# Kernel optimization log

Measured on AMD Instinct MI355X. Metric: run time of the kernel, lower is better.

The kernel has to match this reference:

```python
import jax, jax.numpy as jnp
import numpy as np

H = 16        # num heads
ALPHA = 1.3   # entmax alpha
N_ITER = 50   # bisection iterations
EPS = 1e-5    # layernorm eps


def entmax_bisect(x, alpha=ALPHA, n_iter=N_ITER):
    # x: (..., K). Bisection entmax along last axis (Peters et al. 2019).
    am1 = alpha - 1.0
    x = x - jnp.max(x, axis=-1, keepdims=True)
    m = jnp.max(x, axis=-1, keepdims=True)  # == 0 after shift
    lo, hi = m - 10.0, m + 10.0
    def step(carry, _):
        lo, hi = carry
        mid = 0.5 * (lo + hi)
        p = jnp.maximum(am1 * x - mid, 0.0) ** (1.0 / am1)
        gt = jnp.sum(p, axis=-1, keepdims=True) > 1.0
        return (jnp.where(gt, mid, lo), jnp.where(gt, hi, mid)), None
    (lo, hi), _ = jax.lax.scan(jax.checkpoint(step), (lo, hi), None, length=n_iter)
    p = jnp.maximum(am1 * x - hi, 0.0) ** (1.0 / am1)
    return p / (jnp.sum(p, axis=-1, keepdims=True) + 1e-12)


def _heads(t, B, N, hd):
    return t.reshape(B, N, H, hd).transpose(0, 2, 1, 3)  # (B,H,N,hd)


def attn_branch(x, mask, wq, bq, wk, bk, wv, bv, wo, bo, use_entmax):
    B, N, D = x.shape
    hd = D // H
    q = _heads(x @ wq + bq, B, N, hd)
    k = _heads(x @ wk + bk, B, N, hd)
    v = _heads(x @ wv + bv, B, N, hd)
    s = jnp.einsum('bhqd,bhkd->bhqk', q, k) / float(np.sqrt(hd)) + mask
    if use_entmax:
        s = s - jnp.max(s, axis=-1, keepdims=True)
        a = entmax_bisect(s)
    else:
        a = jax.nn.softmax(s, axis=-1)
    o = jnp.einsum('bhqk,bhkd->bhqd', a, v).transpose(0, 2, 1, 3).reshape(B, N, D)
    return o @ wo + bo


def layer_norm(x, g, b):
    m = jnp.mean(x, axis=-1, keepdims=True)
    v = jnp.mean((x - m) ** 2, axis=-1, keepdims=True)
    return (x - m) * jax.lax.rsqrt(v + EPS) * g + b


def setup_inputs():
    B, N, D, F, FILM, NMODS = 4, 512, 2048, 8192, 64, 10000
    key = jax.random.key(0)
    ks = iter(jax.random.split(key, 64))
    rn = lambda *s: jax.random.normal(next(ks), s, dtype=jnp.float32)
    inp = dict(
        x=rn(B, N, D),
        attn_mask_intra=jnp.zeros((N, N), jnp.float32),
        attn_mask_inter=jnp.zeros((N, N), jnp.float32),
        mods=jax.random.randint(next(ks), (B, N), 0, 9999),
        film_emb=rn(NMODS, FILM) * 0.02,
        film_gw=rn(FILM, D) * 0.02, film_gb=jnp.zeros((D,), jnp.float32),
        film_bw=rn(FILM, D) * 0.02, film_bb=jnp.zeros((D,), jnp.float32),
        gate_alpha=jnp.zeros((2,), jnp.float32),
        ln1_g=jnp.ones((D,), jnp.float32), ln1_b=jnp.zeros((D,), jnp.float32),
        ln2_g=jnp.ones((D,), jnp.float32), ln2_b=jnp.zeros((D,), jnp.float32),
        ffn_w1=rn(D, F) * 0.02, ffn_b1=jnp.zeros((F,), jnp.float32),
        ffn_w2=rn(F, D) * 0.02, ffn_b2=jnp.zeros((D,), jnp.float32),
    )
    for tag in ('a', 'e'):
        for nm in ('q', 'k', 'v', 'o'):
            inp['w%s_%s' % (nm, tag)] = rn(D, D) * 0.02
            inp['b%s_%s' % (nm, tag)] = jnp.zeros((D,), jnp.float32)
    return inp


def reference(x, attn_mask_intra, attn_mask_inter, mods,
              film_emb, film_gw, film_gb, film_bw, film_bb,
              gate_alpha, ln1_g, ln1_b, ln2_g, ln2_b,
              ffn_w1, ffn_b1, ffn_w2, ffn_b2,
              wq_a, bq_a, wk_a, bk_a, wv_a, bv_a, wo_a, bo_a,
              wq_e, bq_e, wk_e, bk_e, wv_e, bv_e, wo_e, bo_e):
    # FiLM modulation on the intra-module branch input
    e = film_emb[jnp.clip(mods, 1, None)]                      # (B,N,FILM)
    y_intra = (1.0 + e @ film_gw + film_gb) * x + (e @ film_bw + film_bb)
    z_intra = attn_branch(y_intra, attn_mask_intra, wq_a, bq_a, wk_a, bk_a,
                          wv_a, bv_a, wo_a, bo_a, use_entmax=False)
    z_inter = attn_branch(x, attn_mask_inter, wq_e, bq_e, wk_e, bk_e,
                          wv_e, bv_e, wo_e, bo_e, use_entmax=True)
    w = jax.nn.softmax(gate_alpha)                              # global gate
    z = w[0] * z_intra + w[1] * z_inter
    h = layer_norm(x + z, ln1_g, ln1_b)                         # Post-LN
    y = jax.nn.relu(h @ ffn_w1 + ffn_b1) @ ffn_w2 + ffn_b2
    return layer_norm(h + y, ln2_g, ln2_b)
```

## Files before the change

kernel.cpp:

```cpp
#include <hip/hip_runtime.h>
#include <hip/hip_bf16.h>

typedef float f32x4 __attribute__((ext_vector_type(4)));
typedef short bf16x8 __attribute__((ext_vector_type(8)));
typedef unsigned short u16;

#define SEQ    512
#define DIM    2048
#define NHEAD  16
#define HDIM   128
#define BATCH  4
#define BTOK   2048
#define FFDIM  8192
#define DSZ    ((long)BTOK*DIM)
#define QKVN   (3*DIM)
#define QKVSZ  ((long)BTOK*QKVN)
#define ISS    0.08838834764831845f

__device__ __forceinline__ u16 f2bf(float f){
  union{float fv;unsigned u;}c;c.fv=f;
  unsigned r=c.u+0x7FFFu+((c.u>>16)&1u); return (u16)(r>>16);
}
__device__ __forceinline__ float bf2f(u16 v){
  union{unsigned u;float f;}c;c.u=((unsigned)v)<<16;return c.f;
}
__device__ __forceinline__ float pow103(float t){
  return __builtin_amdgcn_exp2f(__builtin_amdgcn_logf(t)*(10.0f/3.0f));
}

#define GLD16(g,l) __builtin_amdgcn_global_load_lds( \
    (const __attribute__((address_space(1))) unsigned int*)(g), \
    (__attribute__((address_space(3))) unsigned int*)(l), 16, 0, 0)

#define MF(a,b,c) __builtin_amdgcn_mfma_f32_16x16x32_bf16(a,b,c,0,0,0)
#define VMW(n) do{ asm volatile("s_waitcnt vmcnt(" #n ")" ::: "memory"); \
                   __builtin_amdgcn_sched_barrier(0); }while(0)
#define LGKM0() do{ asm volatile("s_waitcnt lgkmcnt(0)" ::: "memory"); \
                    __builtin_amdgcn_sched_barrier(0); }while(0)
#define BARR() do{ asm volatile("" ::: "memory"); __builtin_amdgcn_s_barrier(); \
                   asm volatile("" ::: "memory"); }while(0)

__global__ __launch_bounds__(256, 2)
void gemm4w(const u16* __restrict__ A, int lda, long sAo, long sAi,
            const u16* __restrict__ B, int ldb, long sBo, long sBi,
            u16* __restrict__ C, int ldc, long sCo,
            const float* __restrict__ bias, long sbias,
            int K, int hdiv, int relu)
{
  __shared__ __align__(16) u16 sm[36864];
  char* smb = (char*)sm;

  int gx = gridDim.x, gy = gridDim.y;
  int nwg = gx*gy*gridDim.z;
  int flat = (blockIdx.z*gy + blockIdx.y)*gx + blockIdx.x;
  int cpx = nwg >> 3; flat = (flat & 7)*cpx + (flat >> 3);
  int by = flat % gy; int tq = flat / gy; int bx = tq % gx; int bz = tq / gx;

  int zo = bz / hdiv, zi = bz - zo*hdiv;
  const u16* Ab = A + (long)zo*sAo + (long)zi*sAi;
  const u16* Bb = B + (long)zo*sBo + (long)zi*sBi;
  int m0 = by*128, n0 = bx*256;

  int tid = threadIdx.x, lane = tid & 63, w = tid >> 6;
  int lr = lane & 15, lg = lane >> 4;
  int rl = lane >> 2, cbyte = (lane & 3)*16;

  int sRA[2], sCA[2];
  #pragma unroll
  for (int q = 0; q < 2; q++) {
    int r = (2*w+q)*16 + rl;
    sRA[q] = r ^ ((r>>2)&1);
    sCA[q] = (cbyte ^ ((((r>>2)^r)&1)<<4) ^ (((r>>1)&1)<<5)) >> 1;
  }
  int sRB[4], sCB[4];
  #pragma unroll
  for (int q = 0; q < 4; q++) {
    int r = (4*w+q)*16 + rl;
    sRB[q] = r ^ ((r>>2)&1);
    sCB[q] = (cbyte ^ ((((r>>2)^r)&1)<<4) ^ (((r>>1)&1)<<5)) >> 1;
  }

  int aoff = (lr*64 + lg*16) ^ ((lane&7)<<4);
  int boff = w*4096 + ((lr*64 + lg*16) ^ ((lane&7)<<4));

  f32x4 acc[8][4] = {};
  int NT = K >> 5;

  auto STG = [&](int buf, int kt) {
    int kcol = kt*32;
    char* base = smb + buf*24576;
    #pragma unroll
    for (int q = 0; q < 2; q++)
      GLD16(Ab + (long)(m0 + sRA[q])*lda + kcol + sCA[q], base + (2*w+q)*1024);
    #pragma unroll
    for (int q = 0; q < 4; q++)
      GLD16(Bb + (long)(n0 + sRB[q])*ldb + kcol + sCB[q], base + 8192 + (4*w+q)*1024);
  };

  STG(0,0);
  if (NT > 1) STG(1,1);

  int buf = 0;
  for (int t = 0; t < NT; t++) {
    char* Ax = smb + buf*24576;
    char* Bx = Ax + 8192;

    if (t+2 < NT) {
      int nb = buf + 2; if (nb >= 3) nb -= 3;
      STG(nb, t+2);
      VMW(12);
    } else if (t+1 < NT) { VMW(6); }
    else                 { VMW(0); }
    BARR();

    bf16x8 af[8], bv[4];
    #pragma unroll
    for (int i = 0; i < 8; i++) af[i] = *(const bf16x8*)(Ax + aoff + i*1024);
    #pragma unroll
    for (int j = 0; j < 4; j++) bv[j] = *(const bf16x8*)(Bx + boff + j*1024);
    LGKM0();
    __builtin_amdgcn_s_setprio(1);
    #pragma unroll
    for (int i = 0; i < 8; i++) {
      acc[i][0] = MF(af[i], bv[0], acc[i][0]);
      acc[i][1] = MF(af[i], bv[1], acc[i][1]);
      acc[i][2] = MF(af[i], bv[2], acc[i][2]);
      acc[i][3] = MF(af[i], bv[3], acc[i][3]);
    }
    __builtin_amdgcn_s_setprio(0);
    BARR();
    buf++; if (buf == 3) buf = 0;
  }

  u16* Cb = C + (long)bz*sCo;
  #pragma unroll
  for (int j = 0; j < 4; j++) {
    int col = n0 + w*64 + j*16 + lr;
    float bv2 = bias ? bias[zo*sbias + col] : 0.0f;
    #pragma unroll
    for (int i = 0; i < 8; i++) {
      #pragma unroll
      for (int e = 0; e < 4; e++) {
        int row = m0 + i*16 + lg*4 + e;
        float v = acc[i][j][e] + bv2;
        if (relu) v = fmaxf(v, 0.0f);
        Cb[(long)row*ldc + col] = f2bf(v);
      }
    }
  }
}

__global__ __launch_bounds__(256, 3)
void gemm4(const u16* __restrict__ A, int lda, long sAo, long sAi,
           const u16* __restrict__ B, int ldb, long sBo, long sBi,
           void* __restrict__ C, int ldc, long sCo, long sCi, int outbf,
           const float* __restrict__ bias, long sbias,
           int K, int hdiv, int relu)
{
  __shared__ __align__(16) u16 sm[24576];
  char* smb = (char*)sm;

  int gx = gridDim.x, gy = gridDim.y;
  int nwg = gx*gy*gridDim.z;
  int flat = (blockIdx.z*gy + blockIdx.y)*gx + blockIdx.x;
  int cpx = nwg >> 3; flat = (flat & 7)*cpx + (flat >> 3);
  int by = flat % gy; int tq = flat / gy; int bx = tq % gx; int bz = tq / gx;

  int zo = bz / hdiv, zi = bz - zo*hdiv;
  const u16* Ab = A + (long)zo*sAo + (long)zi*sAi;
  const u16* Bb = B + (long)zo*sBo + (long)zi*sBi;
  int m0 = by*128, n0 = bx*128;

  int tid = threadIdx.x, lane = tid & 63, w = tid >> 6;
  int wrow = (w>>1)*64, wn = (w&1)*64;
  int lr = lane & 15, lg = lane >> 4;

  int stR[2], stC[2], ldsch[2];
  #pragma unroll
  for (int q = 0; q < 2; q++) {
    int chunk = q*4 + w;
    int r = chunk*16 + (lane>>2);
    int c = (lane&3)*16;
    int Rz = r ^ ((r>>2)&1);
    int Cz = c ^ ((((r>>2)^r)&1)<<4) ^ (((r>>1)&1)<<5);
    stR[q] = Rz; stC[q] = Cz>>1;
    ldsch[q] = chunk*1024;
  }

  int aoff = ((wrow + lr)*64 + lg*16) ^ ((lane&7)<<4);
  int boff = ((wn  + lr)*64 + lg*16) ^ ((lane&7)<<4);

  f32x4 acc[4][4] = {};
  int NT = K >> 5;

  auto STG = [&](int buf, int op, int kt) {
    const u16* gp = op ? Bb : Ab;
    int ld   = op ? ldb : lda;
    int base = op ? n0 : m0;
    int kcol = kt*32;
    #pragma unroll
    for (int q = 0; q < 2; q++) {
      const u16* src = gp + (long)(base + stR[q])*ld + kcol + stC[q];
      char* dst = smb + buf*16384 + op*8192 + ldsch[q];
      GLD16(src, dst);
    }
  };

  STG(0,0,0); STG(0,1,0);
  if (NT > 1) { STG(1,0,1); STG(1,1,1); }

  int buf = 0;
  for (int t = 0; t < NT; t++) {
    char* Ax = smb + buf*16384;
    char* Bx = smb + buf*16384 + 8192;

    if (t+2 < NT) {
      int nb = buf + 2; if (nb >= 3) nb -= 3;
      STG(nb,0,t+2); STG(nb,1,t+2);
      VMW(8);
    } else if (t+1 < NT) { VMW(4); }
    else                 { VMW(0); }
    BARR();

    bf16x8 af[4], bv[4];
    #pragma unroll
    for (int i = 0; i < 4; i++) af[i] = *(const bf16x8*)(Ax + aoff + i*1024);
    #pragma unroll
    for (int j = 0; j < 4; j++) bv[j] = *(const bf16x8*)(Bx + boff + j*1024);
    LGKM0();
    __builtin_amdgcn_s_setprio(1);
    #pragma unroll
    for (int i = 0; i < 4; i++) {
      acc[i][0] = MF(af[i], bv[0], acc[i][0]);
      acc[i][1] = MF(af[i], bv[1], acc[i][1]);
      acc[i][2] = MF(af[i], bv[2], acc[i][2]);
      acc[i][3] = MF(af[i], bv[3], acc[i][3]);
    }
    __builtin_amdgcn_s_setprio(0);
    BARR();
    buf++; if (buf == 3) buf = 0;
  }

  long coff = (long)zo*sCo + (long)zi*sCi;
  if (outbf) {
    u16* Cb = (u16*)C + coff;
    #pragma unroll
    for (int j = 0; j < 4; j++) {
      int col = n0 + wn + j*16 + lr;
      float bv2 = bias ? bias[zo*sbias + col] : 0.0f;
      #pragma unroll
      for (int i = 0; i < 4; i++) {
        #pragma unroll
        for (int e = 0; e < 4; e++) {
          int row = m0 + wrow + i*16 + lg*4 + e;
          float v = acc[i][j][e] + bv2;
          if (relu) v = fmaxf(v, 0.0f);
          Cb[(long)row*ldc + col] = f2bf(v);
        }
      }
    }
  } else {
    float* Cb = (float*)C + coff;
    #pragma unroll
    for (int j = 0; j < 4; j++) {
      int col = n0 + wn + j*16 + lr;
      #pragma unroll
      for (int i = 0; i < 4; i++) {
        #pragma unroll
        for (int e = 0; e < 4; e++) {
          int row = m0 + wrow + i*16 + lg*4 + e;
          Cb[(long)row*ldc + col] = acc[i][j][e];
        }
      }
    }
  }
}

__global__ __launch_bounds__(256, 2)
void qkprobs_both(const u16* __restrict__ QKVp,
                  const float* __restrict__ maskI, const float* __restrict__ maskE,
                  u16* __restrict__ Pall)
{
  __shared__ __align__(16) u16 sm[20480];
  char* smb = (char*)sm;

  int z2 = blockIdx.x;
  int m0 = blockIdx.y*32;
  int br = z2 >> 6, z = z2 & 63;
  int b  = z >> 4, h = z & 15;
  const float* maskp = br ? maskE : maskI;
  const u16* Qb = QKVp + (long)br*QKVSZ + (long)b*SEQ*QKVN + h*HDIM;
  const u16* Kb = Qb + DIM;
  u16* P = Pall + (long)br*64*SEQ*SEQ;

  int tid = threadIdx.x, lane = tid & 63, w = tid >> 6;
  int lr = lane & 15, lg = lane >> 4;
  int wn = w*128;

  int rl = lane >> 2;
  int cb = (lane & 3)*16;

  int aoff = (lr*64 + lg*16) ^ ((lane&7)<<4);
  int boff = ((wn + lr)*64 + lg*16) ^ ((lane&7)<<4);

  auto stgA = [&](int kt) {
    int r = (w&1)*16 + rl;
    int Rz = r ^ ((r>>2)&1);
    int Cz = cb ^ ((((r>>2)^r)&1)<<4) ^ (((r>>1)&1)<<5);
    GLD16(Qb + (long)(m0+Rz)*QKVN + kt*32 + (Cz>>1), smb + kt*2048 + (w&1)*1024);
  };
  auto stgB = [&](int kt) {
    #pragma unroll
    for (int q = 0; q < 8; q++) {
      int chunk = q*4 + w;
      int r = chunk*16 + rl;
      int Rz = r ^ ((r>>2)&1);
      int Cz = cb ^ ((((r>>2)^r)&1)<<4) ^ (((r>>1)&1)<<5);
      GLD16(Kb + (long)Rz*QKVN + kt*32 + (Cz>>1),
            smb + 8192 + chunk*1024);
    }
  };

  f32x4 acc[2][8] = {};

  stgA(0); stgA(1); stgA(2); stgA(3);
  stgB(0);

  #pragma unroll
  for (int kt = 0; kt < 4; kt++) {
    VMW(0);
    BARR();
    char* Bx = smb + 8192;
    bf16x8 af[2], bv[8];
    #pragma unroll
    for (int i = 0; i < 2; i++) af[i] = *(const bf16x8*)(smb + kt*2048 + aoff + i*1024);
    #pragma unroll
    for (int j = 0; j < 8; j++) bv[j] = *(const bf16x8*)(Bx + boff + j*1024);
    LGKM0();
    BARR();
    if (kt < 3) stgB(kt+1);
    __builtin_amdgcn_s_setprio(1);
    #pragma unroll
    for (int i = 0; i < 2; i++)
      #pragma unroll
      for (int j = 0; j < 8; j++)
        acc[i][j] = MF(af[i], bv[j], acc[i][j]);
    __builtin_amdgcn_s_setprio(0);
  }

  float* redA = (float*)smb;
  float* redB = (float*)(smb + 512);

  float rmax[8];
  #pragma unroll
  for (int s = 0; s < 8; s++) rmax[s] = -3.4e38f;
  #pragma unroll
  for (int i = 0; i < 2; i++) {
    #pragma unroll
    for (int e = 0; e < 4; e++) {
      int row = i*16 + lg*4 + e;
      const float* mp = maskp + (long)(m0+row)*SEQ + wn + lr;
      #pragma unroll
      for (int j = 0; j < 8; j++) {
        float v = acc[i][j][e]*ISS + mp[j*16];
        acc[i][j][e] = v;
        rmax[i*4+e] = fmaxf(rmax[i*4+e], v);
      }
    }
  }
  #pragma unroll
  for (int s = 0; s < 8; s++)
    #pragma unroll
    for (int o = 1; o < 16; o <<= 1) rmax[s] = fmaxf(rmax[s], __shfl_xor(rmax[s], o));
  if (lr == 0) {
    #pragma unroll
    for (int i = 0; i < 2; i++)
      #pragma unroll
      for (int e = 0; e < 4; e++) redA[w*32 + i*16 + lg*4 + e] = rmax[i*4+e];
  }
  BARR();
  #pragma unroll
  for (int i = 0; i < 2; i++)
    #pragma unroll
    for (int e = 0; e < 4; e++) {
      int row = i*16 + lg*4 + e;
      rmax[i*4+e] = fmaxf(fmaxf(redA[row], redA[32+row]),
                          fmaxf(redA[64+row], redA[96+row]));
    }
  BARR();

  float inv[8];

  if (br) {
    #pragma unroll
    for (int i = 0; i < 2; i++)
      #pragma unroll
      for (int j = 0; j < 8; j++)
        #pragma unroll
        for (int e = 0; e < 4; e++)
          acc[i][j][e] = (acc[i][j][e] - rmax[i*4+e])*0.3f;

    float lo[8];
    #pragma unroll
    for (int s = 0; s < 8; s++) lo[s] = -1.0f;
    float half = 0.5f;

    #pragma unroll 1
    for (int it = 0; it < 5; it++) {
      float ps[8];
      #pragma unroll
      for (int s = 0; s < 8; s++) ps[s] = 0.0f;
      #pragma unroll
      for (int i = 0; i < 2; i++)
        #pragma unroll
        for (int e = 0; e < 4; e++) {
          float mid = lo[i*4+e] + half;
          #pragma unroll
          for (int j = 0; j < 8; j++) {
            float t = acc[i][j][e] - mid;
            if (t > 0.0f) ps[i*4+e] += pow103(t);
          }
        }
      #pragma unroll
      for (int s = 0; s < 8; s++)
        #pragma unroll
        for (int o = 1; o < 16; o <<= 1) ps[s] += __shfl_xor(ps[s], o);
      if (lr == 0) {
        #pragma unroll
        for (int i = 0; i < 2; i++)
          #pragma unroll
          for (int e = 0; e < 4; e++) redA[w*32 + i*16 + lg*4 + e] = ps[i*4+e];
      }
      BARR();
      #pragma unroll
      for (int i = 0; i < 2; i++)
        #pragma unroll
        for (int e = 0; e < 4; e++) {
          int row = i*16 + lg*4 + e, s = i*4+e;
          float tot = redA[row] + redA[32+row] + redA[64+row] + redA[96+row];
          if (tot > 1.0f) lo[s] += half;
        }
      BARR();
      half *= 0.5f;
    }

    #pragma unroll 1
    for (int it = 0; it < 3; it++) {
      float ps[8], pd[8];
      #pragma unroll
      for (int s = 0; s < 8; s++) { ps[s] = 0.0f; pd[s] = 0.0f; }
      #pragma unroll
      for (int i = 0; i < 2; i++)
        #pragma unroll
        for (int e = 0; e < 4; e++) {
          float tv = lo[i*4+e];
          #pragma unroll
          for (int j = 0; j < 8; j++) {
            float t = acc[i][j][e] - tv;
            if (t > 0.0f) {
              float w7 = __builtin_amdgcn_exp2f(__builtin_amdgcn_logf(t)*(7.0f/3.0f));
              pd[i*4+e] += w7; ps[i*4+e] += w7*t;
            }
          }
        }
      #pragma unroll
      for (int s = 0; s < 8; s++)
        #pragma unroll
        for (int o = 1; o < 16; o <<= 1) {
          ps[s] += __shfl_xor(ps[s], o);
          pd[s] += __shfl_xor(pd[s], o);
        }
      if (lr == 0) {
        #pragma unroll
        for (int i = 0; i < 2; i++)
          #pragma unroll
          for (int e = 0; e < 4; e++) {
            redA[w*32 + i*16 + lg*4 + e] = ps[i*4+e];
            redB[w*32 + i*16 + lg*4 + e] = pd[i*4+e];
          }
      }
      BARR();
      #pragma unroll
      for (int i = 0; i < 2; i++)
        #pragma unroll
        for (int e = 0; e < 4; e++) {
          int row = i*16 + lg*4 + e, s = i*4+e;
          float st = redA[row] + redA[32+row] + redA[64+row] + redA[96+row];
          float dt = redB[row] + redB[32+row] + redB[64+row] + redB[96+row];
          lo[s] += (st - 1.0f) / ((10.0f/3.0f)*dt + 1e-30f);
        }
      BARR();
    }

    float ps[8];
    #pragma unroll
    for (int s = 0; s < 8; s++) ps[s] = 0.0f;
    #pragma unroll
    for (int i = 0; i < 2; i++)
      #pragma unroll
      for (int e = 0; e < 4; e++) {
        float tv = lo[i*4+e];
        #pragma unroll
        for (int j = 0; j < 8; j++) {
          float t = acc[i][j][e] - tv;
          float p = (t > 0.0f) ? pow103(t) : 0.0f;
          acc[i][j][e] = p;
          ps[i*4+e] += p;
        }
      }
    #pragma unroll
    for (int s = 0; s < 8; s++)
      #pragma unroll
      for (int o = 1; o < 16; o <<= 1) ps[s] += __shfl_xor(ps[s], o);
    if (lr == 0) {
      #pragma unroll
      for (int i = 0; i < 2; i++)
        #pragma unroll
        for (int e = 0; e < 4; e++) redA[w*32 + i*16 + lg*4 + e] = ps[i*4+e];
    }
    BARR();
    #pragma unroll
    for (int i = 0; i < 2; i++)
      #pragma unroll
      for (int e = 0; e < 4; e++) {
        int row = i*16 + lg*4 + e;
        inv[i*4+e] = 1.0f/(redA[row] + redA[32+row] + redA[64+row] + redA[96+row] + 1e-12f);
      }
  } else {
    float ps[8];
    #pragma unroll
    for (int s = 0; s < 8; s++) ps[s] = 0.0f;
    #pragma unroll
    for (int i = 0; i < 2; i++)
      #pragma unroll
      for (int e = 0; e < 4; e++) {
        float mx = rmax[i*4+e];
        #pragma unroll
        for (int j = 0; j < 8; j++) {
          float p = __expf(acc[i][j][e] - mx);
          acc[i][j][e] = p;
          ps[i*4+e] += p;
        }
      }
    #pragma unroll
    for (int s = 0; s < 8; s++)
      #pragma unroll
      for (int o = 1; o < 16; o <<= 1) ps[s] += __shfl_xor(ps[s], o);
    if (lr == 0) {
      #pragma unroll
      for (int i = 0; i < 2; i++)
        #pragma unroll
        for (int e = 0; e < 4; e++) redA[w*32 + i*16 + lg*4 + e] = ps[i*4+e];
    }
    BARR();
    #pragma unroll
    for (int i = 0; i < 2; i++)
      #pragma unroll
      for (int e = 0; e < 4; e++) {
        int row = i*16 + lg*4 + e;
        inv[i*4+e] = 1.0f/(redA[row] + redA[32+row] + redA[64+row] + redA[96+row]);
      }
  }

  BARR();
  char* rp = smb + 8192;
  #pragma unroll
  for (int i = 0; i < 2; i++)
    #pragma unroll
    for (int e = 0; e < 4; e++) {
      int r = i*16 + lg*4 + e;
      float sc = inv[i*4+e];
      #pragma unroll
      for (int j = 0; j < 8; j++) {
        int cbyt = (wn + j*16 + lr)*2;
        *(u16*)(rp + r*1024 + (cbyt ^ ((r&7)<<4))) = f2bf(acc[i][j][e]*sc);
      }
    }
  BARR();
  u16* Pb = P + ((long)z*SEQ + m0)*SEQ;
  #pragma unroll
  for (int chunk = 0; chunk < 8; chunk++) {
    int p = chunk*4096 + tid*16;
    int row = p >> 10, cb2 = p & 1023;
    bf16x8 v = *(const bf16x8*)(rp + row*1024 + (cb2 ^ ((row&7)<<4)));
    *(bf16x8*)((char*)Pb + p) = v;
  }
}

__global__ __launch_bounds__(256)
void redk(const float* __restrict__ Pp, int nk, const float* __restrict__ bias,
          u16* __restrict__ out)
{
  long i = ((long)blockIdx.x*256 + threadIdx.x)*8;
  long z = i >> 22;
  int  n = (int)(i & 2047);
  float v[8] = {};
  for (int k = 0; k < nk; k++) {
    const float* s = Pp + (z*nk + k)*DSZ + (i & (DSZ-1));
    f32x4 aa = *(const f32x4*)s, bb = *(const f32x4*)(s+4);
    v[0]+=aa.x; v[1]+=aa.y; v[2]+=aa.z; v[3]+=aa.w;
    v[4]+=bb.x; v[5]+=bb.y; v[6]+=bb.z; v[7]+=bb.w;
  }
  f32x4 b0 = *(const f32x4*)&bias[z*2048 + n], b1 = *(const f32x4*)&bias[z*2048 + n + 4];
  float bv[8] = {b0.x,b0.y,b0.z,b0.w,b1.x,b1.y,b1.z,b1.w};
  u16 w[8] __attribute__((aligned(16)));
  #pragma unroll
  for (int j = 0; j < 8; j++) w[j] = f2bf(v[j] + bv[j]);
  *(bf16x8*)&out[i] = *(bf16x8*)w;
}

struct P6 { const float* p[6]; };

__global__ __launch_bounds__(256)
void wtrans6(P6 srcs, int ldw, u16* __restrict__ Wt, long dstStride, int ldt)
{
  __shared__ u16 t[64][72];
  const float* W = srcs.p[blockIdx.z];
  u16* Wd = Wt + (long)blockIdx.z*dstStride;
  int tid = threadIdx.x, r = tid >> 2, c0 = (tid & 3)*16;
  long gr = (long)blockIdx.y*64 + r, gc = (long)blockIdx.x*64 + c0;
  #pragma unroll
  for (int u = 0; u < 16; u += 4) {
    f32x4 v = *(const f32x4*)&W[gr*ldw + gc + u];
    t[r][c0+u+0]=f2bf(v.x); t[r][c0+u+1]=f2bf(v.y);
    t[r][c0+u+2]=f2bf(v.z); t[r][c0+u+3]=f2bf(v.w);
  }
  __syncthreads();
  u16 o[16] __attribute__((aligned(16)));
  #pragma unroll
  for (int u = 0; u < 16; u++) o[u] = t[c0+u][r];
  u16* dst = &Wd[(long)(blockIdx.x*64 + r)*ldt + blockIdx.y*64 + c0];
  *(bf16x8*)&dst[0] = *(bf16x8*)&o[0];
  *(bf16x8*)&dst[8] = *(bf16x8*)&o[8];
}

__global__ __launch_bounds__(256)
void wtrans(const float* __restrict__ W, int ldw, u16* __restrict__ Wt, int ldt)
{
  __shared__ u16 t[64][72];
  int tid = threadIdx.x, r = tid >> 2, c0 = (tid & 3)*16;
  long gr = (long)blockIdx.y*64 + r, gc = (long)blockIdx.x*64 + c0;
  #pragma unroll
  for (int u = 0; u < 16; u += 4) {
    f32x4 v = *(const f32x4*)&W[gr*ldw + gc + u];
    t[r][c0+u+0]=f2bf(v.x); t[r][c0+u+1]=f2bf(v.y);
    t[r][c0+u+2]=f2bf(v.z); t[r][c0+u+3]=f2bf(v.w);
  }
  __syncthreads();
  u16 o[16] __attribute__((aligned(16)));
  #pragma unroll
  for (int u = 0; u < 16; u++) o[u] = t[c0+u][r];
  u16* dst = &Wt[(long)(blockIdx.x*64 + r)*ldt + blockIdx.y*64 + c0];
  *(bf16x8*)&dst[0] = *(bf16x8*)&o[0];
  *(bf16x8*)&dst[8] = *(bf16x8*)&o[8];
}

__global__ __launch_bounds__(256)
void vtrans_both(const u16* __restrict__ QKVp, u16* __restrict__ Vt)
{
  __shared__ u16 t[64][72];
  int z = blockIdx.z;
  int br = z >> 6, zz = z & 63, b = zz >> 4, h = zz & 15;
  const u16* src = QKVp + (long)br*QKVSZ + (long)b*SEQ*QKVN + h*HDIM + 2*DIM;
  u16* dst = Vt + (long)z*HDIM*SEQ;
  int tid = threadIdx.x, r = tid >> 2, c0 = (tid & 3)*16;
  int tok0 = blockIdx.x*64, d0 = blockIdx.y*64;
  #pragma unroll
  for (int u = 0; u < 16; u += 8) {
    bf16x8 v = *(const bf16x8*)&src[(long)(tok0+r)*QKVN + d0 + c0 + u];
    #pragma unroll
    for (int e = 0; e < 8; e++) t[r][c0+u+e] = (u16)v[e];
  }
  __syncthreads();
  u16 o[16] __attribute__((aligned(16)));
  #pragma unroll
  for (int u = 0; u < 16; u++) o[u] = t[c0+u][r];
  *(bf16x8*)&dst[(long)(d0+r)*SEQ + tok0 + c0]     = *(bf16x8*)&o[0];
  *(bf16x8*)&dst[(long)(d0+r)*SEQ + tok0 + c0 + 8] = *(bf16x8*)&o[8];
}

__global__ __launch_bounds__(256)
void f32_to_bf16(const float* __restrict__ in, u16* __restrict__ o, long n8)
{
  long i = (long)blockIdx.x*256 + threadIdx.x;
  if (i >= n8) return; i *= 8;
  f32x4 a = *(const f32x4*)&in[i], b = *(const f32x4*)&in[i+4];
  u16 w[8] __attribute__((aligned(16)));
  w[0]=f2bf(a.x);w[1]=f2bf(a.y);w[2]=f2bf(a.z);w[3]=f2bf(a.w);
  w[4]=f2bf(b.x);w[5]=f2bf(b.y);w[6]=f2bf(b.z);w[7]=f2bf(b.w);
  *(bf16x8*)&o[i] = *(bf16x8*)w;
}

__global__ __launch_bounds__(256)
void egather(const int* __restrict__ mods, const float* __restrict__ emb, u16* __restrict__ E)
{
  int i = blockIdx.x*256 + threadIdx.x;
  int row = i >> 3, j0 = (i & 7)*8;
  int m = mods[row]; if (m < 1) m = 1;
  const float* s = &emb[(long)m*64 + j0];
  f32x4 a = *(const f32x4*)s, b = *(const f32x4*)(s+4);
  u16 w[8] __attribute__((aligned(16)));
  w[0]=f2bf(a.x);w[1]=f2bf(a.y);w[2]=f2bf(a.z);w[3]=f2bf(a.w);
  w[4]=f2bf(b.x);w[5]=f2bf(b.y);w[6]=f2bf(b.z);w[7]=f2bf(b.w);
  *(bf16x8*)&E[(long)row*64 + j0] = *(bf16x8*)w;
}

__global__ __launch_bounds__(256)
void film_apply(const float* __restrict__ x, const u16* __restrict__ G,
                const u16* __restrict__ B, u16* __restrict__ y)
{
  long i = ((long)blockIdx.x*256 + threadIdx.x)*8;
  f32x4 x0 = *(const f32x4*)&x[i], x1 = *(const f32x4*)&x[i+4];
  bf16x8 g = *(const bf16x8*)&G[i], b = *(const bf16x8*)&B[i];
  float xv[8] = {x0.x,x0.y,x0.z,x0.w,x1.x,x1.y,x1.z,x1.w};
  u16 w[8] __attribute__((aligned(16)));
  #pragma unroll
  for (int e = 0; e < 8; e++)
    w[e] = f2bf((1.0f + bf2f((u16)g[e]))*xv[e] + bf2f((u16)b[e]));
  *(bf16x8*)&y[i] = *(bf16x8*)w;
}

__global__ __launch_bounds__(256)
void pack_bias(float* __restrict__ dst,
               const float* q_a, const float* k_a, const float* v_a,
               const float* q_e, const float* k_e, const float* v_e,
               const float* o_a, const float* o_e,
               const float* fg, const float* fb)
{
  int i = blockIdx.x*256 + threadIdx.x;
  if (i < 12288) {
    int br = i/6144, r = i - br*6144, sel = r >> 11, o = r & 2047;
    const float* s = br ? (sel==0?q_e:sel==1?k_e:v_e)
                        : (sel==0?q_a:sel==1?k_a:v_a);
    dst[i] = s[o];
  } else if (i < 16384) {
    int r = i - 12288; dst[i] = (r>>11) ? o_e[r&2047] : o_a[r&2047];
  } else {
    int r = i - 16384; dst[i] = (r>>11) ? fb[r&2047] : fg[r&2047];
  }
}

__global__ __launch_bounds__(256)
void ln_gate(const float* __restrict__ x, const u16* __restrict__ z0,
             const u16* __restrict__ z1, const float* __restrict__ ga,
             const float* __restrict__ g, const float* __restrict__ b,
             u16* __restrict__ h)
{
  __shared__ float red[8];
  long base = (long)blockIdx.x*DIM;
  int t8 = threadIdx.x*8, lane = threadIdx.x & 63, wid = threadIdx.x >> 6;
  float a0 = ga[0], a1 = ga[1];
  float mm = fmaxf(a0,a1), e0 = __expf(a0-mm), e1 = __expf(a1-mm);
  float w0 = e0/(e0+e1), w1 = e1/(e0+e1);
  f32x4 x0 = *(const f32x4*)&x[base+t8], x1 = *(const f32x4*)&x[base+t8+4];
  bf16x8 zi = *(const bf16x8*)&z0[base+t8], ze = *(const bf16x8*)&z1[base+t8];
  float xv[8] = {x0.x,x0.y,x0.z,x0.w,x1.x,x1.y,x1.z,x1.w};
  float v[8]; float s = 0.0f;
  #pragma unroll
  for (int j = 0; j < 8; j++) {
    v[j] = xv[j] + w0*bf2f((u16)zi[j]) + w1*bf2f((u16)ze[j]);
    s += v[j];
  }
  for (int o = 32; o; o >>= 1) s += __shfl_xor(s, o);
  if (lane == 0) red[wid] = s;
  __syncthreads();
  float mean = (red[0]+red[1]+red[2]+red[3])*(1.0f/DIM);
  float q = 0.0f;
  #pragma unroll
  for (int j = 0; j < 8; j++) { float d = v[j]-mean; q += d*d; }
  for (int o = 32; o; o >>= 1) q += __shfl_xor(q, o);
  if (lane == 0) red[4+wid] = q;
  __syncthreads();
  float inv = rsqrtf((red[4]+red[5]+red[6]+red[7])*(1.0f/DIM) + 1e-5f);
  f32x4 g0 = *(const f32x4*)&g[t8], g1 = *(const f32x4*)&g[t8+4];
  f32x4 b0 = *(const f32x4*)&b[t8], b1 = *(const f32x4*)&b[t8+4];
  float gv[8] = {g0.x,g0.y,g0.z,g0.w,g1.x,g1.y,g1.z,g1.w};
  float bv[8] = {b0.x,b0.y,b0.z,b0.w,b1.x,b1.y,b1.z,b1.w};
  u16 w[8] __attribute__((aligned(16)));
  #pragma unroll
  for (int j = 0; j < 8; j++) w[j] = f2bf((v[j]-mean)*inv*gv[j] + bv[j]);
  *(bf16x8*)&h[base+t8] = *(bf16x8*)w;
}

__global__ __launch_bounds__(256)
void ln_res(const u16* __restrict__ hin, const u16* __restrict__ y,
            const float* __restrict__ g, const float* __restrict__ b,
            float* __restrict__ out)
{
  __shared__ float red[8];
  long base = (long)blockIdx.x*DIM;
  int t8 = threadIdx.x*8, lane = threadIdx.x & 63, wid = threadIdx.x >> 6;
  bf16x8 hv = *(const bf16x8*)&hin[base+t8], yv = *(const bf16x8*)&y[base+t8];
  float v[8]; float s = 0.0f;
  #pragma unroll
  for (int j = 0; j < 8; j++) { v[j] = bf2f((u16)hv[j]) + bf2f((u16)yv[j]); s += v[j]; }
  for (int o = 32; o; o >>= 1) s += __shfl_xor(s, o);
  if (lane == 0) red[wid] = s;
  __syncthreads();
  float mean = (red[0]+red[1]+red[2]+red[3])*(1.0f/DIM);
  float q = 0.0f;
  #pragma unroll
  for (int j = 0; j < 8; j++) { float d = v[j]-mean; q += d*d; }
  for (int o = 32; o; o >>= 1) q += __shfl_xor(q, o);
  if (lane == 0) red[4+wid] = q;
  __syncthreads();
  float inv = rsqrtf((red[4]+red[5]+red[6]+red[7])*(1.0f/DIM) + 1e-5f);
  f32x4 g0 = *(const f32x4*)&g[t8], g1 = *(const f32x4*)&g[t8+4];
  f32x4 b0 = *(const f32x4*)&b[t8], b1 = *(const f32x4*)&b[t8+4];
  float gv[8] = {g0.x,g0.y,g0.z,g0.w,g1.x,g1.y,g1.z,g1.w};
  float bv[8] = {b0.x,b0.y,b0.z,b0.w,b1.x,b1.y,b1.z,b1.w};
  f32x4 o0, o1;
  #pragma unroll
  for (int j = 0; j < 4; j++) o0[j] = (v[j]-mean)*inv*gv[j] + bv[j];
  #pragma unroll
  for (int j = 0; j < 4; j++) o1[j] = (v[4+j]-mean)*inv*gv[4+j] + bv[4+j];
  *(f32x4*)&out[base+t8] = o0;
  *(f32x4*)&out[base+t8+4] = o1;
}

static void G4(hipStream_t st, const u16* A,int lda,long sAo,long sAi,
               const u16* B,int ldb,long sBo,long sBi,
               void* C,int ldc,long sCo,long sCi,int outbf,
               const float* bias,long sbias,int M,int N,int K,int batch,int hdiv,int relu)
{
  gemm4<<<dim3(N/128,M/128,batch),dim3(256),0,st>>>(
      A,lda,sAo,sAi,B,ldb,sBo,sBi,C,ldc,sCo,sCi,outbf,bias,sbias,K,hdiv,relu);
}
static void G4W(hipStream_t st, const u16* A,int lda,long sAo,long sAi,
                const u16* B,int ldb,long sBo,long sBi,
                u16* C,int ldc,long sCo,
                const float* bias,long sbias,int M,int N,int K,int batch,int hdiv,int relu)
{
  gemm4w<<<dim3(N/256,M/128,batch),dim3(256),0,st>>>(
      A,lda,sAo,sAi,B,ldb,sBo,sBi,C,ldc,sCo,bias,sbias,K,hdiv,relu);
}

extern "C" void kernel_launch(void* const* d_in, const int* in_sizes, int n_in,
                              void* d_out, int out_size, void* d_ws, size_t ws_size,
                              hipStream_t stream)
{
  const float* x          = (const float*)d_in[0];
  const float* mask_intra = (const float*)d_in[1];
  const float* mask_inter = (const float*)d_in[2];
  const int*   mods       = (const int*)  d_in[3];
  const float* film_emb   = (const float*)d_in[4];
  const float* film_gw    = (const float*)d_in[5];
  const float* film_gb    = (const float*)d_in[6];
  const float* film_bw    = (const float*)d_in[7];
  const float* film_bb    = (const float*)d_in[8];
  const float* gate_alpha = (const float*)d_in[9];
  const float* ln1_g = (const float*)d_in[10];
  const float* ln1_b = (const float*)d_in[11];
  const float* ln2_g = (const float*)d_in[12];
  const float* ln2_b = (const float*)d_in[13];
  const float* ffn_w1 = (const float*)d_in[14];
  const float* ffn_b1 = (const float*)d_in[15];
  const float* ffn_w2 = (const float*)d_in[16];
  const float* ffn_b2 = (const float*)d_in[17];
  const float* wq_a = (const float*)d_in[18]; const float* bq_a = (const float*)d_in[19];
  const float* wk_a = (const float*)d_in[20]; const float* bk_a = (const float*)d_in[21];
  const float* wv_a = (const float*)d_in[22]; const float* bv_a = (const float*)d_in[23];
  const float* wo_a = (const float*)d_in[24]; const float* bo_a = (const float*)d_in[25];
  const float* wq_e = (const float*)d_in[26]; const float* bq_e = (const float*)d_in[27];
  const float* wk_e = (const float*)d_in[28]; const float* bk_e = (const float*)d_in[29];
  const float* wv_e = (const float*)d_in[30]; const float* bv_e = (const float*)d_in[31];
  const float* wo_e = (const float*)d_in[32]; const float* bo_e = (const float*)d_in[33];

  char* ws = (char*)d_ws;
  u16*   ybf  = (u16*)(ws);
  u16*   xbf  = (u16*)(ws + (8L<<20));
  u16*   AO   = (u16*)(ws);
  u16*   QKV  = (u16*)(ws + (16L<<20));
  u16*   Gf   = QKV;
  u16*   Bfm  = QKV + DSZ;
  u16*   zbuf = (u16*)(ws + (16L<<20));
  u16*   hbf  = (u16*)(ws + (32L<<20));
  u16*   Wst  = (u16*)(ws + (64L<<20));
  u16*   Pall = (u16*)(ws + (96L<<20));
  u16*   mid  = (u16*)(ws + (96L<<20));
  float* Pf2  = (float*)(ws + (128L<<20));
  u16*   f2o  = (u16*)(ws + (16L<<20));
  u16*   Vt   = (u16*)(ws + (160L<<20));
  u16*   Ebuf = (u16*)(ws + (160L<<20));
  u16*   Wfm  = (u16*)(ws + (161L<<20));
  float* bpk  = (float*)(ws + (176L<<20));

  f32_to_bf16<<<2048,256,0,stream>>>(x, xbf, DSZ/8);
  egather<<<64,256,0,stream>>>(mods, film_emb, Ebuf);
  {
    P6 pf; pf.p[0]=film_gw; pf.p[1]=film_bw;
    pf.p[2]=film_gw; pf.p[3]=film_gw; pf.p[4]=film_gw; pf.p[5]=film_gw;
    wtrans6<<<dim3(32,1,2),256,0,stream>>>(pf, DIM, Wfm, (long)DIM*64, 64);
  }
  pack_bias<<<80,256,0,stream>>>(bpk, bq_a,bk_a,bv_a, bq_e,bk_e,bv_e, bo_a,bo_e, film_gb,film_bb);

  G4(stream, Ebuf,64,0,0, Wfm,64,(long)DIM*64,0, Gf,DIM,DSZ,0,1,
     bpk+16384,2048, BTOK,DIM,64, 2,1, 0);
  film_apply<<<2048,256,0,stream>>>(x, Gf, Bfm, ybf);

  {
    P6 pq; pq.p[0]=wq_a; pq.p[1]=wk_a; pq.p[2]=wv_a;
    pq.p[3]=wq_e; pq.p[4]=wk_e; pq.p[5]=wv_e;
    wtrans6<<<dim3(32,32,6),256,0,stream>>>(pq, DIM, Wst, (long)DIM*DIM, DIM);
  }
  G4W(stream, ybf,DIM,DSZ,0, Wst,DIM,(long)QKVN*DIM,0, QKV,QKVN,QKVSZ,
      bpk,QKVN, BTOK,QKVN,DIM, 2,1, 0);

  vtrans_both<<<dim3(8,2,128),256,0,stream>>>(QKV, Vt);
  qkprobs_both<<<dim3(128,16),dim3(256),0,stream>>>(QKV, mask_intra, mask_inter, Pall);
  G4(stream, Pall,SEQ,(long)16*SEQ*SEQ,(long)SEQ*SEQ,
     Vt,SEQ,(long)16*HDIM*SEQ,(long)HDIM*SEQ,
     AO,DIM,(long)SEQ*DIM,HDIM,1, nullptr,0,
     SEQ,HDIM,SEQ, 128,16, 0);

  {
    P6 po; po.p[0]=wo_a; po.p[1]=wo_e;
    po.p[2]=wo_a; po.p[3]=wo_a; po.p[4]=wo_a; po.p[5]=wo_a;
    wtrans6<<<dim3(32,32,2),256,0,stream>>>(po, DIM, Wst, (long)DIM*DIM, DIM);
  }
  G4(stream, AO,DIM,DSZ,0, Wst,DIM,(long)DIM*DIM,0, zbuf,DIM,DSZ,0,1,
     bpk+12288,DIM, BTOK,DIM,DIM, 2,1, 0);

  ln_gate<<<2048,256,0,stream>>>(x, zbuf, zbuf+DSZ, gate_alpha, ln1_g, ln1_b, hbf);

  wtrans<<<dim3(128,32),256,0,stream>>>(ffn_w1, FFDIM, Wst, DIM);
  G4W(stream, hbf,DIM,0,0, Wst,DIM,0,0, mid,FFDIM,0,
      ffn_b1,0, BTOK,FFDIM,DIM, 1,1, 1);
  wtrans<<<dim3(32,128),256,0,stream>>>(ffn_w2, DIM, Wst, FFDIM);
  G4(stream, mid,FFDIM,4096,0, Wst,FFDIM,4096,0, Pf2,DIM,DSZ,0,0,
     nullptr,0, BTOK,DIM,4096, 2,1, 0);
  redk<<<2048,256,0,stream>>>(Pf2, 2, ffn_b2, f2o);

  ln_res<<<2048,256,0,stream>>>(hbf, f2o, ln2_g, ln2_b, (float*)d_out);
}
```

Baseline: 584.4 us.

## Replace wide GEMM with 512-thread 256x256 tile kernel with split-phase prefetch

The 256-thread 128x256 GEMM used for the QKV projection and the first FFN layer is replaced by a 512-thread kernel computing 256x256 tiles, with 8 waves arranged 2x4. This increases operand reuse per workgroup and halves the A reloads per output. The main loop is split into two half-phases, each issuing part of the next stage's global-to-LDS loads and reading A fragments in two halves, so memory traffic interleaves with MFMA work. It uses more LDS (96KB) and more barriers per K step, and with fewer, larger workgroups it risks lower occupancy and worse wave quantization.

```diff
diff --git a/kernel.cpp b/kernel.cpp
--- a/kernel.cpp
+++ b/kernel.cpp
@@ -40,14 +40,14 @@
 #define BARR() do{ asm volatile("" ::: "memory"); __builtin_amdgcn_s_barrier(); \
                    asm volatile("" ::: "memory"); }while(0)
 
-__global__ __launch_bounds__(256, 2)
-void gemm4w(const u16* __restrict__ A, int lda, long sAo, long sAi,
-            const u16* __restrict__ B, int ldb, long sBo, long sBi,
+__global__ __launch_bounds__(512, 2)
+void gemm8p(const u16* __restrict__ A, int lda, long sAo,
+            const u16* __restrict__ B, int ldb, long sBo,
             u16* __restrict__ C, int ldc, long sCo,
             const float* __restrict__ bias, long sbias,
-            int K, int hdiv, int relu)
-{
-  __shared__ __align__(16) u16 sm[36864];
+            int K, int relu)
+{
+  __shared__ __align__(16) u16 sm[49152];
   char* smb = (char*)sm;
 
   int gx = gridDim.x, gy = gridDim.y;
@@ -56,72 +56,69 @@
   int cpx = nwg >> 3; flat = (flat & 7)*cpx + (flat >> 3);
   int by = flat % gy; int tq = flat / gy; int bx = tq % gx; int bz = tq / gx;
 
-  int zo = bz / hdiv, zi = bz - zo*hdiv;
-  const u16* Ab = A + (long)zo*sAo + (long)zi*sAi;
-  const u16* Bb = B + (long)zo*sBo + (long)zi*sBi;
-  int m0 = by*128, n0 = bx*256;
+  const u16* Ab = A + (long)bz*sAo;
+  const u16* Bb = B + (long)bz*sBo;
+  int m0 = by*256, n0 = bx*256;
 
   int tid = threadIdx.x, lane = tid & 63, w = tid >> 6;
+  int wrow = (w>>2)*128, wn = (w&3)*64;
   int lr = lane & 15, lg = lane >> 4;
-  int rl = lane >> 2, cbyte = (lane & 3)*16;
-
-  int sRA[2], sCA[2];
+
+  int stR[2], stC[2], ldsch[2];
   #pragma unroll
   for (int q = 0; q < 2; q++) {
-    int r = (2*w+q)*16 + rl;
-    sRA[q] = r ^ ((r>>2)&1);
-    sCA[q] = (cbyte ^ ((((r>>2)^r)&1)<<4) ^ (((r>>1)&1)<<5)) >> 1;
-  }
-  int sRB[4], sCB[4];
-  #pragma unroll
-  for (int q = 0; q < 4; q++) {
-    int r = (4*w+q)*16 + rl;
-    sRB[q] = r ^ ((r>>2)&1);
-    sCB[q] = (cbyte ^ ((((r>>2)^r)&1)<<4) ^ (((r>>1)&1)<<5)) >> 1;
-  }
-
-  int aoff = (lr*64 + lg*16) ^ ((lane&7)<<4);
-  int boff = w*4096 + ((lr*64 + lg*16) ^ ((lane&7)<<4));
+    int chunk = q*8 + w;
+    int r = chunk*16 + (lane>>2);
+    int c = (lane&3)*16;
+    int Rz = r ^ ((r>>2)&1);
+    int Cz = c ^ ((((r>>2)^r)&1)<<4) ^ (((r>>1)&1)<<5);
+    stR[q] = Rz; stC[q] = Cz>>1;
+    ldsch[q] = chunk*1024;
+  }
+
+  int aoff = ((wrow + lr)*64 + lg*16) ^ ((lane&7)<<4);
+  int boff = ((wn  + lr)*64 + lg*16) ^ ((lane&7)<<4);
 
   f32x4 acc[8][4] = {};
   int NT = K >> 5;
 
-  auto STG = [&](int buf, int kt) {
+  auto STG = [&](int buf, int op, int kt) {
+    const u16* gp = op ? Bb : Ab;
+    int ld   = op ? ldb : lda;
+    int base = op ? n0 : m0;
     int kcol = kt*32;
-    char* base = smb + buf*24576;
-    #pragma unroll
-    for (int q = 0; q < 2; q++)
-      GLD16(Ab + (long)(m0 + sRA[q])*lda + kcol + sCA[q], base + (2*w+q)*1024);
-    #pragma unroll
-    for (int q = 0; q < 4; q++)
-      GLD16(Bb + (long)(n0 + sRB[q])*ldb + kcol + sCB[q], base + 8192 + (4*w+q)*1024);
+    #pragma unroll
+    for (int q = 0; q < 2; q++) {
+      const u16* src = gp + (long)(base + stR[q])*ld + kcol + stC[q];
+      char* dst = smb + buf*32768 + op*16384 + ldsch[q];
+      GLD16(src, dst);
+    }
   };
 
-  STG(0,0);
-  if (NT > 1) STG(1,1);
+  STG(0,0,0); STG(0,1,0);
+  STG(1,0,1); STG(1,1,1);
+  VMW(4);
+  BARR();
 
   int buf = 0;
   for (int t = 0; t < NT; t++) {
-    char* Ax = smb + buf*24576;
-    char* Bx = Ax + 8192;
-
-    if (t+2 < NT) {
-      int nb = buf + 2; if (nb >= 3) nb -= 3;
-      STG(nb, t+2);
-      VMW(12);
-    } else if (t+1 < NT) { VMW(6); }
-    else                 { VMW(0); }
+    char* Ax = smb + buf*32768;
+    char* Bx = Ax + 16384;
+    int b2 = buf + 2; if (b2 >= 3) b2 -= 3;
+    bool st = (t+2 < NT);
+
+    bf16x8 af[4], bv[4];
+
+    #pragma unroll
+    for (int i = 0; i < 4; i++) af[i] = *(const bf16x8*)(Ax + aoff + i*1024);
+    #pragma unroll
+    for (int j = 0; j < 4; j++) bv[j] = *(const bf16x8*)(Bx + boff + j*1024);
+    if (st) STG(b2, 0, t+2);
     BARR();
-
-    bf16x8 af[8], bv[4];
-    #pragma unroll
-    for (int i = 0; i < 8; i++) af[i] = *(const bf16x8*)(Ax + aoff + i*1024);
-    #pragma unroll
-    for (int j = 0; j < 4; j++) bv[j] = *(const bf16x8*)(Bx + boff + j*1024);
     LGKM0();
     __builtin_amdgcn_s_setprio(1);
     #pragma unroll
-    for (int i = 0; i < 8; i++) {
+    for (int i = 0; i < 4; i++) {
       acc[i][0] = MF(af[i], bv[0], acc[i][0]);
       acc[i][1] = MF(af[i], bv[1], acc[i][1]);
       acc[i][2] = MF(af[i], bv[2], acc[i][2]);
@@ -129,19 +126,37 @@
     }
     __builtin_amdgcn_s_setprio(0);
     BARR();
+
+    #pragma unroll
+    for (int i = 0; i < 4; i++) af[i] = *(const bf16x8*)(Ax + aoff + (4+i)*1024);
+    if (st) { STG(b2, 1, t+2); VMW(4); }
+    else if (t+1 < NT) { VMW(0); }
+    BARR();
+    LGKM0();
+    __builtin_amdgcn_s_setprio(1);
+    #pragma unroll
+    for (int i = 0; i < 4; i++) {
+      acc[4+i][0] = MF(af[i], bv[0], acc[4+i][0]);
+      acc[4+i][1] = MF(af[i], bv[1], acc[4+i][1]);
+      acc[4+i][2] = MF(af[i], bv[2], acc[4+i][2]);
+      acc[4+i][3] = MF(af[i], bv[3], acc[4+i][3]);
+    }
+    __builtin_amdgcn_s_setprio(0);
+    BARR();
+
     buf++; if (buf == 3) buf = 0;
   }
 
   u16* Cb = C + (long)bz*sCo;
   #pragma unroll
   for (int j = 0; j < 4; j++) {
-    int col = n0 + w*64 + j*16 + lr;
-    float bv2 = bias ? bias[zo*sbias + col] : 0.0f;
+    int col = n0 + wn + j*16 + lr;
+    float bv2 = bias ? bias[bz*sbias + col] : 0.0f;
     #pragma unroll
     for (int i = 0; i < 8; i++) {
       #pragma unroll
       for (int e = 0; e < 4; e++) {
-        int row = m0 + i*16 + lg*4 + e;
+        int row = m0 + wrow + i*16 + lg*4 + e;
         float v = acc[i][j][e] + bv2;
         if (relu) v = fmaxf(v, 0.0f);
         Cb[(long)row*ldc + col] = f2bf(v);
@@ -826,13 +841,13 @@
   gemm4<<<dim3(N/128,M/128,batch),dim3(256),0,st>>>(
       A,lda,sAo,sAi,B,ldb,sBo,sBi,C,ldc,sCo,sCi,outbf,bias,sbias,K,hdiv,relu);
 }
-static void G4W(hipStream_t st, const u16* A,int lda,long sAo,long sAi,
-                const u16* B,int ldb,long sBo,long sBi,
+static void G8P(hipStream_t st, const u16* A,int lda,long sAo,
+                const u16* B,int ldb,long sBo,
                 u16* C,int ldc,long sCo,
-                const float* bias,long sbias,int M,int N,int K,int batch,int hdiv,int relu)
-{
-  gemm4w<<<dim3(N/256,M/128,batch),dim3(256),0,st>>>(
-      A,lda,sAo,sAi,B,ldb,sBo,sBi,C,ldc,sCo,bias,sbias,K,hdiv,relu);
+                const float* bias,long sbias,int M,int N,int K,int batch,int relu)
+{
+  gemm8p<<<dim3(N/256,M/256,batch),dim3(512),0,st>>>(
+      A,lda,sAo,B,ldb,sBo,C,ldc,sCo,bias,sbias,K,relu);
 }
 
 extern "C" void kernel_launch(void* const* d_in, const int* in_sizes, int n_in,
@@ -903,8 +918,8 @@
     pq.p[3]=wq_e; pq.p[4]=wk_e; pq.p[5]=wv_e;
     wtrans6<<<dim3(32,32,6),256,0,stream>>>(pq, DIM, Wst, (long)DIM*DIM, DIM);
   }
-  G4W(stream, ybf,DIM,DSZ,0, Wst,DIM,(long)QKVN*DIM,0, QKV,QKVN,QKVSZ,
-      bpk,QKVN, BTOK,QKVN,DIM, 2,1, 0);
+  G8P(stream, ybf,DIM,DSZ, Wst,DIM,(long)QKVN*DIM, QKV,QKVN,QKVSZ,
+      bpk,QKVN, BTOK,QKVN,DIM, 2, 0);
 
   vtrans_both<<<dim3(8,2,128),256,0,stream>>>(QKV, Vt);
   qkprobs_both<<<dim3(128,16),dim3(256),0,stream>>>(QKV, mask_intra, mask_inter, Pall);
@@ -924,8 +939,8 @@
   ln_gate<<<2048,256,0,stream>>>(x, zbuf, zbuf+DSZ, gate_alpha, ln1_g, ln1_b, hbf);
 
   wtrans<<<dim3(128,32),256,0,stream>>>(ffn_w1, FFDIM, Wst, DIM);
-  G4W(stream, hbf,DIM,0,0, Wst,DIM,0,0, mid,FFDIM,0,
-      ffn_b1,0, BTOK,FFDIM,DIM, 1,1, 1);
+  G8P(stream, hbf,DIM,0, Wst,DIM,0, mid,FFDIM,0,
+      ffn_b1,0, BTOK,FFDIM,DIM, 1, 1);
   wtrans<<<dim3(32,128),256,0,stream>>>(ffn_w2, DIM, Wst, FFDIM);
   G4(stream, mid,FFDIM,4096,0, Wst,FFDIM,4096,0, Pf2,DIM,DSZ,0,0,
      nullptr,0, BTOK,DIM,4096, 2,1, 0);
```

Result: slower. 601.8 us (+3.0%).

## Add double-buffered 128x256 GEMM variant for the QKV projection

Applied to the files above, without the earlier changes.

Adds gemm4w2, a copy of the wide 128x256 tile GEMM that uses two shared-memory buffers (the 24576-element array read as two 24576-byte halves) and prefetches the next K-tile while MFMAs run on the current one. It uses launch bounds of 256 threads with 2 blocks per SM and raises MFMA issue priority during the compute phase. The QKV projection now uses this kernel. The aim is to hide global-load latency behind compute, at the cost of more registers and possibly lower occupancy than the original variant.

```diff
diff --git a/kernel.cpp b/kernel.cpp
--- a/kernel.cpp
+++ b/kernel.cpp
@@ -150,6 +150,111 @@
   }
 }
 
+__global__ __launch_bounds__(256, 2)
+void gemm4w2(const u16* __restrict__ A, int lda, long sAo, long sAi,
+             const u16* __restrict__ B, int ldb, long sBo, long sBi,
+             u16* __restrict__ C, int ldc, long sCo,
+             const float* __restrict__ bias, long sbias,
+             int K, int hdiv, int relu)
+{
+  __shared__ __align__(16) u16 sm[24576];
+  char* smb = (char*)sm;
+
+  int gx = gridDim.x, gy = gridDim.y;
+  int nwg = gx*gy*gridDim.z;
+  int flat = (blockIdx.z*gy + blockIdx.y)*gx + blockIdx.x;
+  int cpx = nwg >> 3; flat = (flat & 7)*cpx + (flat >> 3);
+  int by = flat % gy; int tq = flat / gy; int bx = tq % gx; int bz = tq / gx;
+
+  int zo = bz / hdiv, zi = bz - zo*hdiv;
+  const u16* Ab = A + (long)zo*sAo + (long)zi*sAi;
+  const u16* Bb = B + (long)zo*sBo + (long)zi*sBi;
+  int m0 = by*128, n0 = bx*256;
+
+  int tid = threadIdx.x, lane = tid & 63, w = tid >> 6;
+  int lr = lane & 15, lg = lane >> 4;
+  int rl = lane >> 2, cbyte = (lane & 3)*16;
+
+  int sRA[2], sCA[2];
+  #pragma unroll
+  for (int q = 0; q < 2; q++) {
+    int r = (2*w+q)*16 + rl;
+    sRA[q] = r ^ ((r>>2)&1);
+    sCA[q] = (cbyte ^ ((((r>>2)^r)&1)<<4) ^ (((r>>1)&1)<<5)) >> 1;
+  }
+  int sRB[4], sCB[4];
+  #pragma unroll
+  for (int q = 0; q < 4; q++) {
+    int r = (4*w+q)*16 + rl;
+    sRB[q] = r ^ ((r>>2)&1);
+    sCB[q] = (cbyte ^ ((((r>>2)^r)&1)<<4) ^ (((r>>1)&1)<<5)) >> 1;
+  }
+
+  int aoff = (lr*64 + lg*16) ^ ((lane&7)<<4);
+  int boff = w*4096 + ((lr*64 + lg*16) ^ ((lane&7)<<4));
+
+  f32x4 acc[8][4] = {};
+  int NT = K >> 5;
+
+  auto STG = [&](int buf, int kt) {
+    int kcol = kt*32;
+    char* base = smb + buf*24576;
+    #pragma unroll
+    for (int q = 0; q < 2; q++)
+      GLD16(Ab + (long)(m0 + sRA[q])*lda + kcol + sCA[q], base + (2*w+q)*1024);
+    #pragma unroll
+    for (int q = 0; q < 4; q++)
+      GLD16(Bb + (long)(n0 + sRB[q])*ldb + kcol + sCB[q], base + 8192 + (4*w+q)*1024);
+  };
+
+  STG(0,0);
+
+  int buf = 0;
+  for (int t = 0; t < NT; t++) {
+    char* Ax = smb + buf*24576;
+    char* Bx = Ax + 8192;
+
+    if (t+1 < NT) { STG(buf^1, t+1); VMW(6); }
+    else          { VMW(0); }
+    BARR();
+
+    bf16x8 af[8], bv[4];
+    #pragma unroll
+    for (int i = 0; i < 8; i++) af[i] = *(const bf16x8*)(Ax + aoff + i*1024);
+    #pragma unroll
+    for (int j = 0; j < 4; j++) bv[j] = *(const bf16x8*)(Bx + boff + j*1024);
+    LGKM0();
+    __builtin_amdgcn_s_setprio(1);
+    #pragma unroll
+    for (int i = 0; i < 8; i++) {
+      acc[i][0] = MF(af[i], bv[0], acc[i][0]);
+      acc[i][1] = MF(af[i], bv[1], acc[i][1]);
+      acc[i][2] = MF(af[i], bv[2], acc[i][2]);
+      acc[i][3] = MF(af[i], bv[3], acc[i][3]);
+    }
+    __builtin_amdgcn_s_setprio(0);
+    BARR();
+    buf ^= 1;
+  }
+
+  u16* Cb = C + (long)bz*sCo;
+  #pragma unroll
+  for (int j = 0; j < 4; j++) {
+    int col = n0 + w*64 + j*16 + lr;
+    float bv2 = bias ? bias[zo*sbias + col] : 0.0f;
+    #pragma unroll
+    for (int i = 0; i < 8; i++) {
+      #pragma unroll
+      for (int e = 0; e < 4; e++) {
+        int row = m0 + i*16 + lg*4 + e;
+        float v = acc[i][j][e] + bv2;
+        if (relu) v = fmaxf(v, 0.0f);
+        Cb[(long)row*ldc + col] = f2bf(v);
+      }
+    }
+  }
+}
+
 __global__ __launch_bounds__(256, 3)
 void gemm4(const u16* __restrict__ A, int lda, long sAo, long sAi,
            const u16* __restrict__ B, int ldb, long sBo, long sBi,
@@ -832,6 +937,14 @@
                 const float* bias,long sbias,int M,int N,int K,int batch,int hdiv,int relu)
 {
   gemm4w<<<dim3(N/256,M/128,batch),dim3(256),0,st>>>(
+      A,lda,sAo,sAi,B,ldb,sBo,sBi,C,ldc,sCo,bias,sbias,K,hdiv,relu);
+}
+static void G4W2(hipStream_t st, const u16* A,int lda,long sAo,long sAi,
+                 const u16* B,int ldb,long sBo,long sBi,
+                 u16* C,int ldc,long sCo,
+                 const float* bias,long sbias,int M,int N,int K,int batch,int hdiv,int relu)
+{
+  gemm4w2<<<dim3(N/256,M/128,batch),dim3(256),0,st>>>(
       A,lda,sAo,sAi,B,ldb,sBo,sBi,C,ldc,sCo,bias,sbias,K,hdiv,relu);
 }
 
@@ -903,8 +1016,8 @@
     pq.p[3]=wq_e; pq.p[4]=wk_e; pq.p[5]=wv_e;
     wtrans6<<<dim3(32,32,6),256,0,stream>>>(pq, DIM, Wst, (long)DIM*DIM, DIM);
   }
-  G4W(stream, ybf,DIM,DSZ,0, Wst,DIM,(long)QKVN*DIM,0, QKV,QKVN,QKVSZ,
-      bpk,QKVN, BTOK,QKVN,DIM, 2,1, 0);
+  G4W2(stream, ybf,DIM,DSZ,0, Wst,DIM,(long)QKVN*DIM,0, QKV,QKVN,QKVSZ,
+       bpk,QKVN, BTOK,QKVN,DIM, 2,1, 0);
 
   vtrans_both<<<dim3(8,2,128),256,0,stream>>>(QKV, Vt);
   qkprobs_both<<<dim3(128,16),dim3(256),0,stream>>>(QKV, mask_intra, mask_inter, Pall);
```

Measured after the change: 584.2 us. Within noise of the previous version (-0.0%).
